# Kernel optimization log

Hardware: AMD Instinct MI355X
Metric: run time of the kernel (lower is better)

Reference implementation:

```python
import jax, jax.numpy as jnp
import numpy as np

N_NODES = 100000
N_EDGES = 3200000
D_IN = 256
D_HID = 256
D_OUT = 64


def setup_inputs() -> dict:
    key = jax.random.key(0)
    k1, k2, k3, k4 = jax.random.split(key, 4)
    x = jax.random.normal(k1, (N_NODES, D_IN), dtype=jnp.float32)
    edge_index = jax.random.randint(k2, (2, N_EDGES), 0, N_NODES, dtype=jnp.int32)
    W1 = jax.random.normal(k3, (D_IN, D_HID), dtype=jnp.float32) / np.sqrt(D_IN)
    b1 = jnp.zeros((D_HID,), dtype=jnp.float32)
    W2 = jax.random.normal(k4, (D_HID, D_OUT), dtype=jnp.float32) / np.sqrt(D_HID)
    b2 = jnp.zeros((D_OUT,), dtype=jnp.float32)
    return {"x": x, "edge_index": edge_index, "W1": W1, "b1": b1, "W2": W2, "b2": b2}


def _gcn_conv(x, src, dst, norm, W, b, n_nodes):
    # dense linear transform, then normalized scatter-add aggregation
    h = x @ W  # [N, out]
    msg = norm[:, None] * h[src]  # gather + scale, [E+N, out]
    out = jax.ops.segment_sum(msg, dst, num_segments=n_nodes)
    return out + b


def reference(x, edge_index, W1, b1, W2, b2):
    n = x.shape[0]
    # add self-loops (PyG GCNConv default)
    loops = jnp.arange(n, dtype=edge_index.dtype)
    src = jnp.concatenate([edge_index[0], loops])
    dst = jnp.concatenate([edge_index[1], loops])
    # symmetric normalization deg^{-1/2}[src] * deg^{-1/2}[dst]
    deg = jax.ops.segment_sum(jnp.ones_like(src, dtype=x.dtype), dst, num_segments=n)
    dinv = jnp.where(deg > 0, jax.lax.rsqrt(jnp.maximum(deg, 1.0)), 0.0)
    norm = dinv[src] * dinv[dst]

    h = _gcn_conv(x, src, dst, norm, W1, b1, n)
    h = jax.nn.relu(h)
    # dropout is identity at inference
    h = _gcn_conv(h, src, dst, norm, W2, b2, n)
    return jax.nn.log_softmax(h, axis=1)
```

## Files before the change

kernel.cpp:

```cpp
#include <hip/hip_runtime.h>
#include <hip/hip_bf16.h>


typedef __bf16 bf16;
typedef bf16 bf16x8 __attribute__((ext_vector_type(8)));
typedef float f32x4 __attribute__((ext_vector_type(4)));
typedef signed char s8;
typedef signed char s8x8 __attribute__((ext_vector_type(8)));

#define NBLK 256

__global__ __launch_bounds__(256) void k_b1(const int* __restrict__ edge, int E, int chunk,
                                            int NB, int* __restrict__ gcnt) {
    __shared__ int cnt[512];
    int tid = threadIdx.x;
    for (int i = tid; i < NB; i += 256) cnt[i] = 0;
    __syncthreads();
    int s = blockIdx.x * chunk, e = min(s + chunk, E);
    for (int i = s + tid; i < e; i += 256) atomicAdd(&cnt[edge[E + i] >> 9], 1);
    __syncthreads();
    for (int i = tid; i < NB; i += 256) gcnt[blockIdx.x * NB + i] = cnt[i];
}

__global__ void k_b2(const int* __restrict__ gcnt, int NB, int E, int* __restrict__ bstart) {
    __shared__ int col[256];
    int k = threadIdx.x;
    int sum = 0;
    if (k < NB)
        for (int b = 0; b < NBLK; ++b) sum += gcnt[b * NB + k];
    col[k] = sum;
    __syncthreads();
    for (int o = 1; o < 256; o <<= 1) {
        int v = (k >= o) ? col[k - o] : 0;
        __syncthreads();
        col[k] += v;
        __syncthreads();
    }
    if (k < NB) bstart[k] = col[k] - sum;
    if (k == 0) bstart[NB] = E;
}

__global__ void k_b2b(int* __restrict__ gcnt, int NB, const int* __restrict__ bstart) {
    __shared__ int col[256];
    int b = threadIdx.x;
    int k = blockIdx.x;
    int v = gcnt[b * NB + k];
    col[b] = v;
    __syncthreads();
    for (int o = 1; o < 256; o <<= 1) {
        int t = (b >= o) ? col[b - o] : 0;
        __syncthreads();
        col[b] += t;
        __syncthreads();
    }
    gcnt[b * NB + k] = bstart[k] + col[b] - v;
}

__global__ __launch_bounds__(256) void k_b3(const int* __restrict__ edge, int E, int chunk,
                                            int NB, const int* __restrict__ base,
                                            int* __restrict__ ebuf) {
    __shared__ int cnt[512];
    __shared__ int bs[512];
    int tid = threadIdx.x;
    for (int i = tid; i < NB; i += 256) {
        cnt[i] = 0;
        bs[i] = base[blockIdx.x * NB + i];
    }
    __syncthreads();
    int s = blockIdx.x * chunk, e = min(s + chunk, E);
    for (int i = s + tid; i < e; i += 256) {
        int sv = edge[i], dv = edge[E + i];
        int k = dv >> 9;
        int r = atomicAdd(&cnt[k], 1);
        ebuf[bs[k] + r] = sv | ((dv & 511) << 17);
    }
}

__global__ __launch_bounds__(256) void k_b4(const int* __restrict__ ebuf,
                                            const int* __restrict__ bstart, int n,
                                            int* __restrict__ deg) {
    __shared__ int cnt[512];
    int tid = threadIdx.x;
    int k = blockIdx.x;
    cnt[tid] = 0;
    cnt[tid + 256] = 0;
    __syncthreads();
    int s = bstart[k], e = bstart[k + 1];
    for (int i = s + tid; i < e; i += 256) atomicAdd(&cnt[(ebuf[i] >> 17) & 511], 1);
    __syncthreads();
    int base = k << 9;
    if (base + tid < n) deg[base + tid] = cnt[tid];
    if (base + 256 + tid < n) deg[base + 256 + tid] = cnt[tid + 256];
}

__global__ void k_scan1(const int* __restrict__ deg, int n, int* __restrict__ bsum) {
    __shared__ int red[256];
    int base = blockIdx.x * 1024;
    int tid = threadIdx.x;
    int s = 0;
#pragma unroll
    for (int j = 0; j < 4; ++j) {
        int i = base + j * 256 + tid;
        if (i < n) s += deg[i];
    }
    red[tid] = s;
    __syncthreads();
    for (int o = 128; o > 0; o >>= 1) {
        if (tid < o) red[tid] += red[tid + o];
        __syncthreads();
    }
    if (tid == 0) bsum[blockIdx.x] = red[0];
}

__global__ void k_scan2(int* __restrict__ bsum, int nb, int E, int* __restrict__ off, int n) {
    if (threadIdx.x == 0) {
        int run = 0;
        for (int b = 0; b < nb; ++b) { int v = bsum[b]; bsum[b] = run; run += v; }
        off[n] = E;
    }
}

__global__ void k_scan3(const int* __restrict__ deg, int n, const int* __restrict__ bbase,
                        int* __restrict__ off, float* __restrict__ dinv) {
    __shared__ int red[256];
    int base = blockIdx.x * 1024;
    int tid = threadIdx.x;
    int d[4], t = 0;
#pragma unroll
    for (int j = 0; j < 4; ++j) {
        int i = base + tid * 4 + j;
        d[j] = (i < n) ? deg[i] : 0;
        t += d[j];
    }
    red[tid] = t;
    __syncthreads();
    for (int o = 1; o < 256; o <<= 1) {
        int v = (tid >= o) ? red[tid - o] : 0;
        __syncthreads();
        red[tid] += v;
        __syncthreads();
    }
    int run = bbase[blockIdx.x] + red[tid] - t;
#pragma unroll
    for (int j = 0; j < 4; ++j) {
        int i = base + tid * 4 + j;
        if (i < n) {
            off[i] = run;
            dinv[i] = rsqrtf((float)(d[j] + 1));
            run += d[j];
        }
    }
}

__global__ __launch_bounds__(256) void k_b6(const int* __restrict__ ebuf,
                                            const int* __restrict__ bstart,
                                            const int* __restrict__ off,
                                            const float* __restrict__ dinv, int n,
                                            int2* __restrict__ pair) {
    __shared__ int cnt[512];
    __shared__ int offl[512];
    int tid = threadIdx.x;
    int k = blockIdx.x;
    int base = k << 9;
    cnt[tid] = 0;
    cnt[tid + 256] = 0;
    offl[tid] = (base + tid < n) ? off[base + tid] : 0;
    offl[tid + 256] = (base + 256 + tid < n) ? off[base + 256 + tid] : 0;
    __syncthreads();
    int s = bstart[k], e = bstart[k + 1];
    for (int i = s + tid; i < e; i += 256) {
        int pk = ebuf[i];
        int sv = pk & 0x1ffff;
        int node = (pk >> 17) & 511;
        int r = atomicAdd(&cnt[node], 1);
        pair[offl[node] + r] = make_int2(sv, __float_as_int(dinv[sv]));
    }
}

__global__ __launch_bounds__(256) void k_quant(const float* __restrict__ x,
                                               s8* __restrict__ xq,
                                               float* __restrict__ scale, int n) {
    int row = blockIdx.x * 4 + (threadIdx.x >> 6);
    int lane = threadIdx.x & 63;
    if (row >= n) return;
    f32x4 v = ((const f32x4*)x)[(size_t)row * 64 + lane];
    float m = fmaxf(fmaxf(fabsf(v[0]), fabsf(v[1])), fmaxf(fabsf(v[2]), fabsf(v[3])));
    for (int o = 32; o > 0; o >>= 1) m = fmaxf(m, __shfl_xor(m, o));
    m = fmaxf(m, 1e-20f);
    float inv = 127.0f / m;
    int b0 = __float2int_rn(v[0] * inv) & 255;
    int b1 = __float2int_rn(v[1] * inv) & 255;
    int b2 = __float2int_rn(v[2] * inv) & 255;
    int b3 = __float2int_rn(v[3] * inv) & 255;
    ((int*)xq)[(size_t)row * 64 + lane] = b0 | (b1 << 8) | (b2 << 16) | (b3 << 24);
    if (lane == 0) scale[row] = m / 127.0f;
}

__global__ __launch_bounds__(256) void k_quant2(const bf16* __restrict__ tb,
                                                s8* __restrict__ tq,
                                                float* __restrict__ tscale, int n) {
    int t = blockIdx.x * 256 + threadIdx.x;
    int row = t >> 3;
    int l8 = t & 7;
    if (row >= n) return;
    bf16x8 v = ((const bf16x8*)tb)[(size_t)row * 8 + l8];
    float f[8], m = 0.0f;
#pragma unroll
    for (int j = 0; j < 8; ++j) { f[j] = (float)v[j]; m = fmaxf(m, fabsf(f[j])); }
    for (int o = 4; o > 0; o >>= 1) m = fmaxf(m, __shfl_xor(m, o));
    m = fmaxf(m, 1e-20f);
    float inv = 127.0f / m;
    int lo = 0, hi = 0;
#pragma unroll
    for (int j = 0; j < 4; ++j) lo |= (__float2int_rn(f[j] * inv) & 255) << (8 * j);
#pragma unroll
    for (int j = 0; j < 4; ++j) hi |= (__float2int_rn(f[4 + j] * inv) & 255) << (8 * j);
    ((int2*)tq)[(size_t)row * 8 + l8] = make_int2(lo, hi);
    if (l8 == 0) tscale[row] = m / 127.0f;
}

__global__ void k_wt(const float* __restrict__ W, bf16* __restrict__ Wt, int NC) {
    int nc = blockIdx.x;
    int k = threadIdx.x;
    Wt[nc * 256 + k] = (bf16)W[k * NC + nc];
}

__global__ __launch_bounds__(256) void k_agg1(const s8* __restrict__ xq,
                                              const float* __restrict__ scale,
                                              const int* __restrict__ off,
                                              const int2* __restrict__ pair,
                                              const float* __restrict__ dinv,
                                              bf16* __restrict__ ax, int n) {
    int wv = blockIdx.x * 4 + (threadIdx.x >> 6);
    int lane = threadIdx.x & 63;
    int node = wv * 2 + (lane >> 5);
    int l32 = lane & 31;
    if (node >= n) return;
    int s0 = off[node], s1 = off[node + 1];
    float dv = dinv[node];
    const s8x8* X = (const s8x8*)xq;
    s8x8 xs = X[(size_t)node * 32 + l32];
    float ws = dv * scale[node];
    float a[8];
#pragma unroll
    for (int j = 0; j < 8; ++j) a[j] = ws * (float)xs[j];
    int e = s0;
    for (; e + 8 <= s1; e += 8) {
        int2 p[8];
#pragma unroll
        for (int q = 0; q < 8; ++q) p[q] = pair[e + q];
        float sc[8];
#pragma unroll
        for (int q = 0; q < 8; ++q) sc[q] = scale[p[q].x];
        s8x8 t[8];
#pragma unroll
        for (int q = 0; q < 8; ++q) t[q] = X[(size_t)p[q].x * 32 + l32];
#pragma unroll
        for (int q = 0; q < 8; ++q) {
            float w = __int_as_float(p[q].y) * sc[q];
#pragma unroll
            for (int j = 0; j < 8; ++j) a[j] += w * (float)t[q][j];
        }
    }
    for (; e < s1; ++e) {
        int2 p = pair[e];
        float w = __int_as_float(p.y) * scale[p.x];
        s8x8 t = X[(size_t)p.x * 32 + l32];
#pragma unroll
        for (int j = 0; j < 8; ++j) a[j] += w * (float)t[j];
    }
    bf16x8 o;
#pragma unroll
    for (int j = 0; j < 8; ++j) o[j] = (bf16)(a[j] * dv);
    ((bf16x8*)ax)[(size_t)node * 32 + l32] = o;
}

template <bool BIAS_RELU>
__global__ __launch_bounds__(256) void k_gemm(const bf16* __restrict__ A,
                                              const bf16* __restrict__ Bt,
                                              const float* __restrict__ bias,
                                              bf16* __restrict__ C, int n, int NC) {
    __shared__ __align__(16) bf16 As[4 * 64 * 8];
    __shared__ __align__(16) bf16 Bs[4 * 64 * 8];
    int tid = threadIdx.x;
    int bm = blockIdx.x * 64;
    int bn = blockIdx.y * 64;
    int w = tid >> 6, lane = tid & 63;
    int wm = w >> 1, wn = w & 1;

    int r = tid >> 2;
    int cq = tid & 3;
    int lds_idx = (((r >> 4) * 64) + cq * 16 + (r & 15)) * 8;
    int arow = bm + r; if (arow > n - 1) arow = n - 1;
    int brow = bn + r;

    f32x4 acc[2][2] = {};

    for (int k0 = 0; k0 < 256; k0 += 32) {
        __syncthreads();
        uint4 av = *(const uint4*)(A + (size_t)arow * 256 + k0 + cq * 8);
        uint4 bv = *(const uint4*)(Bt + (size_t)brow * 256 + k0 + cq * 8);
        *(uint4*)(As + lds_idx) = av;
        *(uint4*)(Bs + lds_idx) = bv;
        __syncthreads();
#pragma unroll
        for (int i = 0; i < 2; ++i) {
            bf16x8 af = *(const bf16x8*)(As + ((wm * 2 + i) * 64 + lane) * 8);
#pragma unroll
            for (int j = 0; j < 2; ++j) {
                bf16x8 bfr = *(const bf16x8*)(Bs + ((wn * 2 + j) * 64 + lane) * 8);
                acc[i][j] = __builtin_amdgcn_mfma_f32_16x16x32_bf16(af, bfr, acc[i][j], 0, 0, 0);
            }
        }
    }

    int colb = lane & 15, rowq = lane >> 4;
#pragma unroll
    for (int i = 0; i < 2; ++i) {
#pragma unroll
        for (int j = 0; j < 2; ++j) {
            int col = bn + wn * 32 + j * 16 + colb;
#pragma unroll
            for (int rr = 0; rr < 4; ++rr) {
                int row = bm + wm * 32 + i * 16 + rowq * 4 + rr;
                if (row < n) {
                    float v = acc[i][j][rr];
                    if constexpr (BIAS_RELU) {
                        v += bias[col];
                        v = v > 0.0f ? v : 0.0f;
                    }
                    C[(size_t)row * NC + col] = (bf16)v;
                }
            }
        }
    }
}

__global__ __launch_bounds__(256) void k_agg2(const s8* __restrict__ tq,
                                              const float* __restrict__ tscale,
                                              const int* __restrict__ off,
                                              const int2* __restrict__ pair,
                                              const float* __restrict__ dinv,
                                              const float* __restrict__ b2,
                                              float* __restrict__ out, int n) {
    int wv = blockIdx.x * 4 + (threadIdx.x >> 6);
    int lane = threadIdx.x & 63;
    int node = wv * 8 + (lane >> 3);
    int l8 = lane & 7;
    if (node >= n) return;
    int s0 = off[node], s1 = off[node + 1];
    float dv = dinv[node];
    const s8x8* T = (const s8x8*)tq;
    s8x8 ts = T[(size_t)node * 8 + l8];
    float ws = dv * tscale[node];
    float a[8];
#pragma unroll
    for (int j = 0; j < 8; ++j) a[j] = ws * (float)ts[j];
    int e = s0;
    for (; e + 4 <= s1; e += 4) {
        int2 p[4];
#pragma unroll
        for (int q = 0; q < 4; ++q) p[q] = pair[e + q];
        float sc[4];
#pragma unroll
        for (int q = 0; q < 4; ++q) sc[q] = tscale[p[q].x];
        s8x8 tv[4];
#pragma unroll
        for (int q = 0; q < 4; ++q) tv[q] = T[(size_t)p[q].x * 8 + l8];
#pragma unroll
        for (int q = 0; q < 4; ++q) {
            float w = __int_as_float(p[q].y) * sc[q];
#pragma unroll
            for (int j = 0; j < 8; ++j) a[j] += w * (float)tv[q][j];
        }
    }
    for (; e < s1; ++e) {
        int2 p = pair[e];
        float w = __int_as_float(p.y) * tscale[p.x];
        s8x8 tv = T[(size_t)p.x * 8 + l8];
#pragma unroll
        for (int j = 0; j < 8; ++j) a[j] += w * (float)tv[j];
    }
    const float4* B2 = (const float4*)b2;
    float4 bv0 = B2[l8 * 2], bv1 = B2[l8 * 2 + 1];
    a[0] = a[0] * dv + bv0.x; a[1] = a[1] * dv + bv0.y;
    a[2] = a[2] * dv + bv0.z; a[3] = a[3] * dv + bv0.w;
    a[4] = a[4] * dv + bv1.x; a[5] = a[5] * dv + bv1.y;
    a[6] = a[6] * dv + bv1.z; a[7] = a[7] * dv + bv1.w;
    float m = a[0];
#pragma unroll
    for (int j = 1; j < 8; ++j) m = fmaxf(m, a[j]);
    for (int o = 4; o > 0; o >>= 1) m = fmaxf(m, __shfl_xor(m, o));
    float s = 0.0f;
#pragma unroll
    for (int j = 0; j < 8; ++j) s += __expf(a[j] - m);
    for (int o = 4; o > 0; o >>= 1) s += __shfl_xor(s, o);
    float ls = m + __logf(s);
    f32x4 o0, o1;
    o0[0] = a[0] - ls; o0[1] = a[1] - ls; o0[2] = a[2] - ls; o0[3] = a[3] - ls;
    o1[0] = a[4] - ls; o1[1] = a[5] - ls; o1[2] = a[6] - ls; o1[3] = a[7] - ls;
    f32x4* O = (f32x4*)out;
    O[(size_t)node * 16 + l8 * 2] = o0;
    O[(size_t)node * 16 + l8 * 2 + 1] = o1;
}

extern "C" void kernel_launch(void* const* d_in, const int* in_sizes, int n_in,
                              void* d_out, int out_size, void* d_ws, size_t ws_size,
                              hipStream_t stream) {
    const float* x   = (const float*)d_in[0];
    const int*  edge = (const int*)d_in[1];
    const float* W1  = (const float*)d_in[2];
    const float* b1  = (const float*)d_in[3];
    const float* W2  = (const float*)d_in[4];
    const float* b2  = (const float*)d_in[5];
    float* out = (float*)d_out;

    int n = in_sizes[0] / 256;
    int E = in_sizes[1] / 2;
    int nb = (n + 1023) / 1024;
    int NB = (n + 511) >> 9;
    int chunk = (E + NBLK - 1) / NBLK;

    char* ws = (char*)d_ws;
    auto alloc = [&](size_t bytes) -> char* {
        char* p = ws;
        ws += (bytes + 255) & ~(size_t)255;
        return p;
    };
    int*   gcnt   = (int*)alloc((size_t)NBLK * NB * 4);
    int*   bstart = (int*)alloc((size_t)(NB + 1) * 4);
    int*   ebuf   = (int*)alloc((size_t)E * 4);
    int*   deg    = (int*)alloc((size_t)n * 4);
    float* dinv   = (float*)alloc((size_t)n * 4);
    int*   off    = (int*)alloc((size_t)(n + 1) * 4);
    int*   bsum   = (int*)alloc((size_t)nb * 4);
    int2*  pair   = (int2*)alloc((size_t)E * 8);
    s8*    xq     = (s8*)alloc((size_t)n * 256);
    float* scale  = (float*)alloc((size_t)n * 4);
    bf16*  ax     = (bf16*)alloc((size_t)n * 256 * 2);
    bf16*  h1     = (bf16*)alloc((size_t)n * 256 * 2);
    bf16*  tb     = (bf16*)alloc((size_t)n * 64 * 2);
    s8*    tq     = (s8*)alloc((size_t)n * 64);
    float* tscale = (float*)alloc((size_t)n * 4);
    bf16*  W1t    = (bf16*)alloc(256 * 256 * 2);
    bf16*  W2t    = (bf16*)alloc(64 * 256 * 2);

    k_b1<<<NBLK, 256, 0, stream>>>(edge, E, chunk, NB, gcnt);
    k_b2<<<1, 256, 0, stream>>>(gcnt, NB, E, bstart);
    k_b2b<<<NB, 256, 0, stream>>>(gcnt, NB, bstart);
    k_b3<<<NBLK, 256, 0, stream>>>(edge, E, chunk, NB, gcnt, ebuf);
    k_b4<<<NB, 256, 0, stream>>>(ebuf, bstart, n, deg);
    k_scan1<<<nb, 256, 0, stream>>>(deg, n, bsum);
    k_scan2<<<1, 64, 0, stream>>>(bsum, nb, E, off, n);
    k_scan3<<<nb, 256, 0, stream>>>(deg, n, bsum, off, dinv);
    k_b6<<<NB, 256, 0, stream>>>(ebuf, bstart, off, dinv, n, pair);

    k_quant<<<(n + 3) / 4, 256, 0, stream>>>(x, xq, scale, n);
    k_wt<<<256, 256, 0, stream>>>(W1, W1t, 256);
    k_wt<<<64, 256, 0, stream>>>(W2, W2t, 64);

    k_agg1<<<(n + 7) / 8, 256, 0, stream>>>(xq, scale, off, pair, dinv, ax, n);
    dim3 g1((n + 63) / 64, 4);
    k_gemm<true><<<g1, 256, 0, stream>>>(ax, W1t, b1, h1, n, 256);

    dim3 g2((n + 63) / 64, 1);
    k_gemm<false><<<g2, 256, 0, stream>>>(h1, W2t, nullptr, tb, n, 64);
    k_quant2<<<(n * 8 + 255) / 256, 256, 0, stream>>>(tb, tq, tscale, n);
    k_agg2<<<(n + 31) / 32, 256, 0, stream>>>(tq, tscale, off, pair, dinv, b2, out, n);
}
```

Baseline: 559.9 us.

## Split layer-1 aggregation into feature-slab passes and shrink CSR edge records

The int8 feature matrix is stored as eight column slabs of 32 bytes per node. Layer-1 aggregation then runs as eight passes, one per slab, so each pass gathers from a 3.2 MB table that may stay in cache instead of the full 25.6 MB. The CSR edge list now holds only source indices, and the per-source dinv is folded into the quantization scale, which halves the edge stream and drops one multiply per edge. The cost is that the edge list and offsets are re-read eight times, with eight launches and narrower 4-byte gathers per lane.

```diff
diff --git a/kernel.cpp b/kernel.cpp
--- a/kernel.cpp
+++ b/kernel.cpp
@@ -3,10 +3,12 @@
 
 
 typedef __bf16 bf16;
+typedef bf16 bf16x4 __attribute__((ext_vector_type(4)));
 typedef bf16 bf16x8 __attribute__((ext_vector_type(8)));
 typedef float f32x4 __attribute__((ext_vector_type(4)));
 typedef signed char s8;
-typedef signed char s8x8 __attribute__((ext_vector_type(8)));
+typedef s8 s8x4 __attribute__((ext_vector_type(4)));
+typedef s8 s8x8 __attribute__((ext_vector_type(8)));
 
 #define NBLK 256
 
@@ -154,9 +156,8 @@
 
 __global__ __launch_bounds__(256) void k_b6(const int* __restrict__ ebuf,
                                             const int* __restrict__ bstart,
-                                            const int* __restrict__ off,
-                                            const float* __restrict__ dinv, int n,
-                                            int2* __restrict__ pair) {
+                                            const int* __restrict__ off, int n,
+                                            int* __restrict__ csr_src) {
     __shared__ int cnt[512];
     __shared__ int offl[512];
     int tid = threadIdx.x;
@@ -170,16 +171,16 @@
     int s = bstart[k], e = bstart[k + 1];
     for (int i = s + tid; i < e; i += 256) {
         int pk = ebuf[i];
-        int sv = pk & 0x1ffff;
         int node = (pk >> 17) & 511;
         int r = atomicAdd(&cnt[node], 1);
-        pair[offl[node] + r] = make_int2(sv, __float_as_int(dinv[sv]));
+        csr_src[offl[node] + r] = pk & 0x1ffff;
     }
 }
 
 __global__ __launch_bounds__(256) void k_quant(const float* __restrict__ x,
-                                               s8* __restrict__ xq,
-                                               float* __restrict__ scale, int n) {
+                                               const float* __restrict__ dinv,
+                                               s8* __restrict__ xqc,
+                                               float* __restrict__ wsrc, int n) {
     int row = blockIdx.x * 4 + (threadIdx.x >> 6);
     int lane = threadIdx.x & 63;
     if (row >= n) return;
@@ -192,13 +193,16 @@
     int b1 = __float2int_rn(v[1] * inv) & 255;
     int b2 = __float2int_rn(v[2] * inv) & 255;
     int b3 = __float2int_rn(v[3] * inv) & 255;
-    ((int*)xq)[(size_t)row * 64 + lane] = b0 | (b1 << 8) | (b2 << 16) | (b3 << 24);
-    if (lane == 0) scale[row] = m / 127.0f;
+    int f = lane >> 3;
+    int pos = (lane & 7) * 4;
+    *(int*)(xqc + ((size_t)f * n + row) * 32 + pos) = b0 | (b1 << 8) | (b2 << 16) | (b3 << 24);
+    if (lane == 0) wsrc[row] = (m / 127.0f) * dinv[row];
 }
 
 __global__ __launch_bounds__(256) void k_quant2(const bf16* __restrict__ tb,
+                                                const float* __restrict__ dinv,
                                                 s8* __restrict__ tq,
-                                                float* __restrict__ tscale, int n) {
+                                                float* __restrict__ tw, int n) {
     int t = blockIdx.x * 256 + threadIdx.x;
     int row = t >> 3;
     int l8 = t & 7;
@@ -216,7 +220,7 @@
 #pragma unroll
     for (int j = 0; j < 4; ++j) hi |= (__float2int_rn(f[4 + j] * inv) & 255) << (8 * j);
     ((int2*)tq)[(size_t)row * 8 + l8] = make_int2(lo, hi);
-    if (l8 == 0) tscale[row] = m / 127.0f;
+    if (l8 == 0) tw[row] = (m / 127.0f) * dinv[row];
 }
 
 __global__ void k_wt(const float* __restrict__ W, bf16* __restrict__ Wt, int NC) {
@@ -225,54 +229,52 @@
     Wt[nc * 256 + k] = (bf16)W[k * NC + nc];
 }
 
-__global__ __launch_bounds__(256) void k_agg1(const s8* __restrict__ xq,
-                                              const float* __restrict__ scale,
-                                              const int* __restrict__ off,
-                                              const int2* __restrict__ pair,
-                                              const float* __restrict__ dinv,
-                                              bf16* __restrict__ ax, int n) {
-    int wv = blockIdx.x * 4 + (threadIdx.x >> 6);
-    int lane = threadIdx.x & 63;
-    int node = wv * 2 + (lane >> 5);
-    int l32 = lane & 31;
+__global__ __launch_bounds__(256) void k_agg1p(const s8* __restrict__ xsub,
+                                               const float* __restrict__ wsrc,
+                                               const int* __restrict__ off,
+                                               const int* __restrict__ csr_src,
+                                               const float* __restrict__ dinv,
+                                               bf16* __restrict__ ax, int n, int fbase) {
+    int t = blockIdx.x * 256 + threadIdx.x;
+    int node = t >> 3;
+    int l8 = t & 7;
     if (node >= n) return;
     int s0 = off[node], s1 = off[node + 1];
     float dv = dinv[node];
-    const s8x8* X = (const s8x8*)xq;
-    s8x8 xs = X[(size_t)node * 32 + l32];
-    float ws = dv * scale[node];
-    float a[8];
-#pragma unroll
-    for (int j = 0; j < 8; ++j) a[j] = ws * (float)xs[j];
+    const s8x4* X = (const s8x4*)xsub;
+    s8x4 xs = X[(size_t)node * 8 + l8];
+    float wn = wsrc[node];
+    float a[4];
+#pragma unroll
+    for (int j = 0; j < 4; ++j) a[j] = wn * (float)xs[j];
     int e = s0;
     for (; e + 8 <= s1; e += 8) {
-        int2 p[8];
-#pragma unroll
-        for (int q = 0; q < 8; ++q) p[q] = pair[e + q];
-        float sc[8];
-#pragma unroll
-        for (int q = 0; q < 8; ++q) sc[q] = scale[p[q].x];
-        s8x8 t[8];
-#pragma unroll
-        for (int q = 0; q < 8; ++q) t[q] = X[(size_t)p[q].x * 32 + l32];
+        int sv[8];
+#pragma unroll
+        for (int q = 0; q < 8; ++q) sv[q] = __builtin_nontemporal_load(csr_src + e + q);
+        float w[8];
+#pragma unroll
+        for (int q = 0; q < 8; ++q) w[q] = wsrc[sv[q]];
+        s8x4 xv[8];
+#pragma unroll
+        for (int q = 0; q < 8; ++q) xv[q] = X[(size_t)sv[q] * 8 + l8];
 #pragma unroll
         for (int q = 0; q < 8; ++q) {
-            float w = __int_as_float(p[q].y) * sc[q];
-#pragma unroll
-            for (int j = 0; j < 8; ++j) a[j] += w * (float)t[q][j];
+#pragma unroll
+            for (int j = 0; j < 4; ++j) a[j] += w[q] * (float)xv[q][j];
         }
     }
     for (; e < s1; ++e) {
-        int2 p = pair[e];
-        float w = __int_as_float(p.y) * scale[p.x];
-        s8x8 t = X[(size_t)p.x * 32 + l32];
-#pragma unroll
-        for (int j = 0; j < 8; ++j) a[j] += w * (float)t[j];
-    }
-    bf16x8 o;
-#pragma unroll
-    for (int j = 0; j < 8; ++j) o[j] = (bf16)(a[j] * dv);
-    ((bf16x8*)ax)[(size_t)node * 32 + l32] = o;
+        int sv = __builtin_nontemporal_load(csr_src + e);
+        float w = wsrc[sv];
+        s8x4 xv = X[(size_t)sv * 8 + l8];
+#pragma unroll
+        for (int j = 0; j < 4; ++j) a[j] += w * (float)xv[j];
+    }
+    bf16x4 o;
+#pragma unroll
+    for (int j = 0; j < 4; ++j) o[j] = (bf16)(a[j] * dv);
+    __builtin_nontemporal_store(o, (bf16x4*)(ax + (size_t)node * 256 + fbase + l8 * 4));
 }
 
 template <bool BIAS_RELU>
@@ -337,9 +339,9 @@
 }
 
 __global__ __launch_bounds__(256) void k_agg2(const s8* __restrict__ tq,
-                                              const float* __restrict__ tscale,
+                                              const float* __restrict__ tw,
                                               const int* __restrict__ off,
-                                              const int2* __restrict__ pair,
+                                              const int* __restrict__ csr_src,
                                               const float* __restrict__ dinv,
                                               const float* __restrict__ b2,
                                               float* __restrict__ out, int n) {
@@ -352,32 +354,31 @@
     float dv = dinv[node];
     const s8x8* T = (const s8x8*)tq;
     s8x8 ts = T[(size_t)node * 8 + l8];
-    float ws = dv * tscale[node];
+    float ws = tw[node];
     float a[8];
 #pragma unroll
     for (int j = 0; j < 8; ++j) a[j] = ws * (float)ts[j];
     int e = s0;
     for (; e + 4 <= s1; e += 4) {
-        int2 p[4];
-#pragma unroll
-        for (int q = 0; q < 4; ++q) p[q] = pair[e + q];
-        float sc[4];
-#pragma unroll
-        for (int q = 0; q < 4; ++q) sc[q] = tscale[p[q].x];
+        int sv[4];
+#pragma unroll
+        for (int q = 0; q < 4; ++q) sv[q] = __builtin_nontemporal_load(csr_src + e + q);
+        float w[4];
+#pragma unroll
+        for (int q = 0; q < 4; ++q) w[q] = tw[sv[q]];
         s8x8 tv[4];
 #pragma unroll
-        for (int q = 0; q < 4; ++q) tv[q] = T[(size_t)p[q].x * 8 + l8];
+        for (int q = 0; q < 4; ++q) tv[q] = T[(size_t)sv[q] * 8 + l8];
 #pragma unroll
         for (int q = 0; q < 4; ++q) {
-            float w = __int_as_float(p[q].y) * sc[q];
-#pragma unroll
-            for (int j = 0; j < 8; ++j) a[j] += w * (float)tv[q][j];
+#pragma unroll
+            for (int j = 0; j < 8; ++j) a[j] += w[q] * (float)tv[q][j];
         }
     }
     for (; e < s1; ++e) {
-        int2 p = pair[e];
-        float w = __int_as_float(p.y) * tscale[p.x];
-        s8x8 tv = T[(size_t)p.x * 8 + l8];
+        int sv = __builtin_nontemporal_load(csr_src + e);
+        float w = tw[sv];
+        s8x8 tv = T[(size_t)sv * 8 + l8];
 #pragma unroll
         for (int j = 0; j < 8; ++j) a[j] += w * (float)tv[j];
     }
@@ -427,23 +428,23 @@
         ws += (bytes + 255) & ~(size_t)255;
         return p;
     };
-    int*   gcnt   = (int*)alloc((size_t)NBLK * NB * 4);
-    int*   bstart = (int*)alloc((size_t)(NB + 1) * 4);
-    int*   ebuf   = (int*)alloc((size_t)E * 4);
-    int*   deg    = (int*)alloc((size_t)n * 4);
-    float* dinv   = (float*)alloc((size_t)n * 4);
-    int*   off    = (int*)alloc((size_t)(n + 1) * 4);
-    int*   bsum   = (int*)alloc((size_t)nb * 4);
-    int2*  pair   = (int2*)alloc((size_t)E * 8);
-    s8*    xq     = (s8*)alloc((size_t)n * 256);
-    float* scale  = (float*)alloc((size_t)n * 4);
-    bf16*  ax     = (bf16*)alloc((size_t)n * 256 * 2);
-    bf16*  h1     = (bf16*)alloc((size_t)n * 256 * 2);
-    bf16*  tb     = (bf16*)alloc((size_t)n * 64 * 2);
-    s8*    tq     = (s8*)alloc((size_t)n * 64);
-    float* tscale = (float*)alloc((size_t)n * 4);
-    bf16*  W1t    = (bf16*)alloc(256 * 256 * 2);
-    bf16*  W2t    = (bf16*)alloc(64 * 256 * 2);
+    int*   gcnt    = (int*)alloc((size_t)NBLK * NB * 4);
+    int*   bstart  = (int*)alloc((size_t)(NB + 1) * 4);
+    int*   ebuf    = (int*)alloc((size_t)E * 4);
+    int*   deg     = (int*)alloc((size_t)n * 4);
+    float* dinv    = (float*)alloc((size_t)n * 4);
+    int*   off     = (int*)alloc((size_t)(n + 1) * 4);
+    int*   bsum    = (int*)alloc((size_t)nb * 4);
+    int*   csr_src = (int*)alloc((size_t)E * 4);
+    s8*    xqc     = (s8*)alloc((size_t)n * 256);
+    float* wsrc    = (float*)alloc((size_t)n * 4);
+    bf16*  ax      = (bf16*)alloc((size_t)n * 256 * 2);
+    bf16*  h1      = (bf16*)alloc((size_t)n * 256 * 2);
+    bf16*  tb      = (bf16*)alloc((size_t)n * 64 * 2);
+    s8*    tq      = (s8*)alloc((size_t)n * 64);
+    float* tw      = (float*)alloc((size_t)n * 4);
+    bf16*  W1t     = (bf16*)alloc(256 * 256 * 2);
+    bf16*  W2t     = (bf16*)alloc(64 * 256 * 2);
 
     k_b1<<<NBLK, 256, 0, stream>>>(edge, E, chunk, NB, gcnt);
     k_b2<<<1, 256, 0, stream>>>(gcnt, NB, E, bstart);
@@ -453,18 +454,22 @@
     k_scan1<<<nb, 256, 0, stream>>>(deg, n, bsum);
     k_scan2<<<1, 64, 0, stream>>>(bsum, nb, E, off, n);
     k_scan3<<<nb, 256, 0, stream>>>(deg, n, bsum, off, dinv);
-    k_b6<<<NB, 256, 0, stream>>>(ebuf, bstart, off, dinv, n, pair);
-
-    k_quant<<<(n + 3) / 4, 256, 0, stream>>>(x, xq, scale, n);
+    k_b6<<<NB, 256, 0, stream>>>(ebuf, bstart, off, n, csr_src);
+
+    k_quant<<<(n + 3) / 4, 256, 0, stream>>>(x, dinv, xqc, wsrc, n);
     k_wt<<<256, 256, 0, stream>>>(W1, W1t, 256);
     k_wt<<<64, 256, 0, stream>>>(W2, W2t, 64);
 
-    k_agg1<<<(n + 7) / 8, 256, 0, stream>>>(xq, scale, off, pair, dinv, ax, n);
+    int g1p = (n * 8 + 255) / 256;
+    for (int f = 0; f < 8; ++f) {
+        k_agg1p<<<g1p, 256, 0, stream>>>(xqc + (size_t)f * n * 32, wsrc, off, csr_src,
+                                         dinv, ax, n, f * 32);
+    }
     dim3 g1((n + 63) / 64, 4);
     k_gemm<true><<<g1, 256, 0, stream>>>(ax, W1t, b1, h1, n, 256);
 
     dim3 g2((n + 63) / 64, 1);
     k_gemm<false><<<g2, 256, 0, stream>>>(h1, W2t, nullptr, tb, n, 64);
-    k_quant2<<<(n * 8 + 255) / 256, 256, 0, stream>>>(tb, tq, tscale, n);
-    k_agg2<<<(n + 31) / 32, 256, 0, stream>>>(tq, tscale, off, pair, dinv, b2, out, n);
-}
+    k_quant2<<<(n * 8 + 255) / 256, 256, 0, stream>>>(tb, dinv, tq, tw, n);
+    k_agg2<<<(n + 31) / 32, 256, 0, stream>>>(tq, tw, off, csr_src, dinv, b2, out, n);
+}
```

New measurement: 898.1 us. 60.4% more time.

## Fuse degree count with bucket-local scan and widen first GEMM to full rows

Applied to the files above, without the earlier changes.

The degree histogram kernel now computes the exclusive prefix sum within each 512-node bucket and writes CSR offsets and dinv directly. Bucket start offsets already equal global edge offsets, which removes three scan kernels and the deg/bsum buffers. The first GEMM now has each block compute all 256 output columns for 64 rows with 16 accumulators per wave. This reads each A tile once instead of four times, at the cost of more registers and a larger B staging load per k-step.

```diff
diff --git a/kernel.cpp b/kernel.cpp
--- a/kernel.cpp
+++ b/kernel.cpp
@@ -3,10 +3,11 @@
 
 
 typedef __bf16 bf16;
+typedef bf16 bf16x4 __attribute__((ext_vector_type(4)));
 typedef bf16 bf16x8 __attribute__((ext_vector_type(8)));
 typedef float f32x4 __attribute__((ext_vector_type(4)));
 typedef signed char s8;
-typedef signed char s8x8 __attribute__((ext_vector_type(8)));
+typedef s8 s8x8 __attribute__((ext_vector_type(8)));
 
 #define NBLK 256
 
@@ -76,10 +77,12 @@
     }
 }
 
-__global__ __launch_bounds__(256) void k_b4(const int* __restrict__ ebuf,
-                                            const int* __restrict__ bstart, int n,
-                                            int* __restrict__ deg) {
+__global__ __launch_bounds__(256) void k_b45(const int* __restrict__ ebuf,
+                                             const int* __restrict__ bstart, int n, int E,
+                                             int NB, int* __restrict__ off,
+                                             float* __restrict__ dinv) {
     __shared__ int cnt[512];
+    __shared__ int red[256];
     int tid = threadIdx.x;
     int k = blockIdx.x;
     cnt[tid] = 0;
@@ -88,51 +91,9 @@
     int s = bstart[k], e = bstart[k + 1];
     for (int i = s + tid; i < e; i += 256) atomicAdd(&cnt[(ebuf[i] >> 17) & 511], 1);
     __syncthreads();
-    int base = k << 9;
-    if (base + tid < n) deg[base + tid] = cnt[tid];
-    if (base + 256 + tid < n) deg[base + 256 + tid] = cnt[tid + 256];
-}
-
-__global__ void k_scan1(const int* __restrict__ deg, int n, int* __restrict__ bsum) {
-    __shared__ int red[256];
-    int base = blockIdx.x * 1024;
-    int tid = threadIdx.x;
-    int s = 0;
-#pragma unroll
-    for (int j = 0; j < 4; ++j) {
-        int i = base + j * 256 + tid;
-        if (i < n) s += deg[i];
-    }
-    red[tid] = s;
-    __syncthreads();
-    for (int o = 128; o > 0; o >>= 1) {
-        if (tid < o) red[tid] += red[tid + o];
-        __syncthreads();
-    }
-    if (tid == 0) bsum[blockIdx.x] = red[0];
-}
-
-__global__ void k_scan2(int* __restrict__ bsum, int nb, int E, int* __restrict__ off, int n) {
-    if (threadIdx.x == 0) {
-        int run = 0;
-        for (int b = 0; b < nb; ++b) { int v = bsum[b]; bsum[b] = run; run += v; }
-        off[n] = E;
-    }
-}
-
-__global__ void k_scan3(const int* __restrict__ deg, int n, const int* __restrict__ bbase,
-                        int* __restrict__ off, float* __restrict__ dinv) {
-    __shared__ int red[256];
-    int base = blockIdx.x * 1024;
-    int tid = threadIdx.x;
-    int d[4], t = 0;
-#pragma unroll
-    for (int j = 0; j < 4; ++j) {
-        int i = base + tid * 4 + j;
-        d[j] = (i < n) ? deg[i] : 0;
-        t += d[j];
-    }
-    red[tid] = t;
+    int c0 = cnt[tid * 2], c1 = cnt[tid * 2 + 1];
+    int sum = c0 + c1;
+    red[tid] = sum;
     __syncthreads();
     for (int o = 1; o < 256; o <<= 1) {
         int v = (tid >= o) ? red[tid - o] : 0;
@@ -140,16 +101,15 @@
         red[tid] += v;
         __syncthreads();
     }
-    int run = bbase[blockIdx.x] + red[tid] - t;
-#pragma unroll
-    for (int j = 0; j < 4; ++j) {
-        int i = base + tid * 4 + j;
-        if (i < n) {
-            off[i] = run;
-            dinv[i] = rsqrtf((float)(d[j] + 1));
-            run += d[j];
-        }
-    }
+    int ex = red[tid] - sum;
+    int base = k << 9;
+    int g0 = base + tid * 2, g1 = g0 + 1;
+    int o0 = s + ex, o1 = s + ex + c0;
+    if (g0 < n) { off[g0] = o0; dinv[g0] = rsqrtf((float)(c0 + 1)); }
+    else if (g0 == n) off[g0] = o0;
+    if (g1 < n) { off[g1] = o1; dinv[g1] = rsqrtf((float)(c1 + 1)); }
+    else if (g1 == n) off[g1] = o1;
+    if (k == NB - 1 && tid == 0) off[n] = E;
 }
 
 __global__ __launch_bounds__(256) void k_b6(const int* __restrict__ ebuf,
@@ -275,16 +235,65 @@
     ((bf16x8*)ax)[(size_t)node * 32 + l32] = o;
 }
 
-template <bool BIAS_RELU>
-__global__ __launch_bounds__(256) void k_gemm(const bf16* __restrict__ A,
-                                              const bf16* __restrict__ Bt,
-                                              const float* __restrict__ bias,
-                                              bf16* __restrict__ C, int n, int NC) {
+__global__ __launch_bounds__(256) void k_gemmp(const bf16* __restrict__ A,
+                                               const bf16* __restrict__ Bt,
+                                               const float* __restrict__ bias,
+                                               bf16* __restrict__ C, int n) {
+    __shared__ __align__(16) bf16 As[4 * 64 * 8];
+    __shared__ __align__(16) bf16 Bs[16 * 64 * 8];
+    int tid = threadIdx.x;
+    int bm = blockIdx.x * 64;
+    int w = tid >> 6, lane = tid & 63;
+
+    int r = tid >> 2;
+    int cq = tid & 3;
+    int a_idx = (((r >> 4) * 64) + cq * 16 + (r & 15)) * 8;
+    int arow = bm + r; if (arow > n - 1) arow = n - 1;
+
+    f32x4 acc[16] = {};
+
+    for (int k0 = 0; k0 < 256; k0 += 32) {
+        __syncthreads();
+        uint4 av = *(const uint4*)(A + (size_t)arow * 256 + k0 + cq * 8);
+        *(uint4*)(As + a_idx) = av;
+#pragma unroll
+        for (int rep = 0; rep < 4; ++rep) {
+            int r2 = rep * 64 + r;
+            uint4 bv = *(const uint4*)(Bt + (size_t)r2 * 256 + k0 + cq * 8);
+            *(uint4*)(Bs + (((r2 >> 4) * 64) + cq * 16 + (r2 & 15)) * 8) = bv;
+        }
+        __syncthreads();
+        bf16x8 af = *(const bf16x8*)(As + (w * 64 + lane) * 8);
+#pragma unroll
+        for (int ct = 0; ct < 16; ++ct) {
+            bf16x8 bfr = *(const bf16x8*)(Bs + (ct * 64 + lane) * 8);
+            acc[ct] = __builtin_amdgcn_mfma_f32_16x16x32_bf16(af, bfr, acc[ct], 0, 0, 0);
+        }
+    }
+
+    int colb = lane & 15, rowq = lane >> 4;
+#pragma unroll
+    for (int ct = 0; ct < 16; ++ct) {
+        int col = ct * 16 + colb;
+        float bv = bias[col];
+#pragma unroll
+        for (int rr = 0; rr < 4; ++rr) {
+            int row = bm + w * 16 + rowq * 4 + rr;
+            if (row < n) {
+                float v = acc[ct][rr] + bv;
+                C[(size_t)row * 256 + col] = (bf16)(v > 0.0f ? v : 0.0f);
+            }
+        }
+    }
+}
+
+__global__ __launch_bounds__(256) void k_gemm2(const bf16* __restrict__ A,
+                                               const bf16* __restrict__ Bt,
+                                               bf16* __restrict__ C, int n) {
     __shared__ __align__(16) bf16 As[4 * 64 * 8];
     __shared__ __align__(16) bf16 Bs[4 * 64 * 8];
     int tid = threadIdx.x;
     int bm = blockIdx.x * 64;
-    int bn = blockIdx.y * 64;
     int w = tid >> 6, lane = tid & 63;
     int wm = w >> 1, wn = w & 1;
 
@@ -292,14 +301,13 @@
     int cq = tid & 3;
     int lds_idx = (((r >> 4) * 64) + cq * 16 + (r & 15)) * 8;
     int arow = bm + r; if (arow > n - 1) arow = n - 1;
-    int brow = bn + r;
 
     f32x4 acc[2][2] = {};
 
     for (int k0 = 0; k0 < 256; k0 += 32) {
         __syncthreads();
         uint4 av = *(const uint4*)(A + (size_t)arow * 256 + k0 + cq * 8);
-        uint4 bv = *(const uint4*)(Bt + (size_t)brow * 256 + k0 + cq * 8);
+        uint4 bv = *(const uint4*)(Bt + (size_t)r * 256 + k0 + cq * 8);
         *(uint4*)(As + lds_idx) = av;
         *(uint4*)(Bs + lds_idx) = bv;
         __syncthreads();
@@ -319,18 +327,11 @@
     for (int i = 0; i < 2; ++i) {
 #pragma unroll
         for (int j = 0; j < 2; ++j) {
-            int col = bn + wn * 32 + j * 16 + colb;
+            int col = wn * 32 + j * 16 + colb;
 #pragma unroll
             for (int rr = 0; rr < 4; ++rr) {
                 int row = bm + wm * 32 + i * 16 + rowq * 4 + rr;
-                if (row < n) {
-                    float v = acc[i][j][rr];
-                    if constexpr (BIAS_RELU) {
-                        v += bias[col];
-                        v = v > 0.0f ? v : 0.0f;
-                    }
-                    C[(size_t)row * NC + col] = (bf16)v;
-                }
+                if (row < n) C[(size_t)row * 64 + col] = (bf16)acc[i][j][rr];
             }
         }
     }
@@ -417,7 +418,6 @@
 
     int n = in_sizes[0] / 256;
     int E = in_sizes[1] / 2;
-    int nb = (n + 1023) / 1024;
     int NB = (n + 511) >> 9;
     int chunk = (E + NBLK - 1) / NBLK;
 
@@ -430,10 +430,8 @@
     int*   gcnt   = (int*)alloc((size_t)NBLK * NB * 4);
     int*   bstart = (int*)alloc((size_t)(NB + 1) * 4);
     int*   ebuf   = (int*)alloc((size_t)E * 4);
-    int*   deg    = (int*)alloc((size_t)n * 4);
     float* dinv   = (float*)alloc((size_t)n * 4);
     int*   off    = (int*)alloc((size_t)(n + 1) * 4);
-    int*   bsum   = (int*)alloc((size_t)nb * 4);
     int2*  pair   = (int2*)alloc((size_t)E * 8);
     s8*    xq     = (s8*)alloc((size_t)n * 256);
     float* scale  = (float*)alloc((size_t)n * 4);
@@ -449,10 +447,7 @@
     k_b2<<<1, 256, 0, stream>>>(gcnt, NB, E, bstart);
     k_b2b<<<NB, 256, 0, stream>>>(gcnt, NB, bstart);
     k_b3<<<NBLK, 256, 0, stream>>>(edge, E, chunk, NB, gcnt, ebuf);
-    k_b4<<<NB, 256, 0, stream>>>(ebuf, bstart, n, deg);
-    k_scan1<<<nb, 256, 0, stream>>>(deg, n, bsum);
-    k_scan2<<<1, 64, 0, stream>>>(bsum, nb, E, off, n);
-    k_scan3<<<nb, 256, 0, stream>>>(deg, n, bsum, off, dinv);
+    k_b45<<<NB, 256, 0, stream>>>(ebuf, bstart, n, E, NB, off, dinv);
     k_b6<<<NB, 256, 0, stream>>>(ebuf, bstart, off, dinv, n, pair);
 
     k_quant<<<(n + 3) / 4, 256, 0, stream>>>(x, xq, scale, n);
@@ -460,11 +455,9 @@
     k_wt<<<64, 256, 0, stream>>>(W2, W2t, 64);
 
     k_agg1<<<(n + 7) / 8, 256, 0, stream>>>(xq, scale, off, pair, dinv, ax, n);
-    dim3 g1((n + 63) / 64, 4);
-    k_gemm<true><<<g1, 256, 0, stream>>>(ax, W1t, b1, h1, n, 256);
-
-    dim3 g2((n + 63) / 64, 1);
-    k_gemm<false><<<g2, 256, 0, stream>>>(h1, W2t, nullptr, tb, n, 64);
+    k_gemmp<<<(n + 63) / 64, 256, 0, stream>>>(ax, W1t, b1, h1, n);
+
+    k_gemm2<<<(n + 63) / 64, 256, 0, stream>>>(h1, W2t, tb, n);
     k_quant2<<<(n * 8 + 255) / 256, 256, 0, stream>>>(tb, tq, tscale, n);
     k_agg2<<<(n + 31) / 32, 256, 0, stream>>>(tq, tscale, off, pair, dinv, b2, out, n);
 }
```

Result: no change. 553.5 us (-1.1%).
